# Optimization experiments

Measured on AMD Instinct MI355X. Metric: run time of the kernel, lower is better.

The kernel has to match this reference:

```python
import jax, jax.numpy as jnp
import numpy as np

HEADS = 16
KV_HEADS = 8
HEAD_DIM = 128
ROPE_BASE = 10000.0
RMS_EPS = 1e-5


def rmsnorm(x, w, eps=RMS_EPS):
    x = jnp.clip(x.astype(jnp.float32), -100.0, 100.0)
    var = jnp.clip(jnp.mean(x * x, axis=-1, keepdims=True), eps, None)
    x = x * jax.lax.rsqrt(var + eps)
    x = jnp.clip(x, -10.0, 10.0)
    return w * x


def activation_quant(x):
    x = jnp.clip(x, -50.0, 50.0)
    max_val = jnp.clip(jnp.max(jnp.abs(x), axis=-1, keepdims=True), 0.0001, None)
    scale = 127.0 / max_val
    return jnp.clip(jnp.round(x * scale), -128.0, 127.0) / scale


def weight_quant(w):
    scale = jnp.clip(jnp.mean(jnp.abs(w)), 1e-8, None)
    e = jnp.mean(w)
    return jnp.sign(w - e) * scale


def bitlinear(x, w, norm_w):
    xn = rmsnorm(x, norm_w)
    xq = xn + jax.lax.stop_gradient(activation_quant(xn) - xn)
    wq = w + jax.lax.stop_gradient(weight_quant(w) - w)
    return xq @ wq.T


def rope_tables(seq_len, dim):
    inv_freq = 1.0 / (ROPE_BASE ** (jnp.arange(0, dim, 2, dtype=jnp.float32) / dim))
    freqs = jnp.outer(jnp.arange(seq_len, dtype=jnp.float32), inv_freq)  # [S, dim/2]
    emb = jnp.concatenate([freqs, freqs], axis=-1)  # [S, dim]
    return jnp.cos(emb), jnp.sin(emb)


def rotate_half(x):
    x1, x2 = jnp.split(x, 2, axis=-1)
    return jnp.concatenate([-x2, x1], axis=-1)


def attention_forward(hidden_states, attention_mask, wq, wk, wv, wo, nq, nk, nv, no):
    B, S, H = hidden_states.shape
    q = bitlinear(hidden_states, wq, nq)  # [B,S,nh*hd]
    k = bitlinear(hidden_states, wk, nk)  # [B,S,nkv*hd]
    v = bitlinear(hidden_states, wv, nv)

    q = q.reshape(B, S, HEADS, HEAD_DIM).transpose(0, 2, 1, 3)       # [B,nh,S,hd]
    k = k.reshape(B, S, KV_HEADS, HEAD_DIM).transpose(0, 2, 1, 3)    # [B,nkv,S,hd]
    v = v.reshape(B, S, KV_HEADS, HEAD_DIM).transpose(0, 2, 1, 3)

    cos, sin = rope_tables(S, HEAD_DIM)
    cos = cos[None, None]  # [1,1,S,hd]
    sin = sin[None, None]
    q = q * cos + rotate_half(q) * sin
    k = k * cos + rotate_half(k) * sin

    groups = HEADS // KV_HEADS
    k_exp = jnp.repeat(k, groups, axis=1)  # [B,nh,S,hd]
    v_exp = jnp.repeat(v, groups, axis=1)

    scale = 1.0 / jnp.sqrt(jnp.float32(HEAD_DIM))
    scores = jnp.einsum('bhqd,bhkd->bhqk', q, k_exp) * scale
    scores = scores + attention_mask
    attn = jax.nn.softmax(scores, axis=-1)
    out = jnp.einsum('bhqk,bhkd->bhqd', attn, v_exp)
    out = out.transpose(0, 2, 1, 3).reshape(B, S, HEADS * HEAD_DIM)
    return bitlinear(out, wo, no)


def setup_inputs() -> dict:
    key = jax.random.key(0)
    ks = jax.random.split(key, 6)
    B, S, H = 2, 2048, 2048
    KVH = KV_HEADS * HEAD_DIM
    std = 0.02 / np.sqrt(H)
    return {
        'hidden_states': jax.random.normal(ks[0], (B, S, H), jnp.float32),
        'attention_mask': jnp.zeros((1, 1, S, S), jnp.float32),
        'wq': jax.random.normal(ks[1], (H, H), jnp.float32) * std,
        'wk': jax.random.normal(ks[2], (KVH, H), jnp.float32) * std,
        'wv': jax.random.normal(ks[3], (KVH, H), jnp.float32) * std,
        'wo': jax.random.normal(ks[4], (H, H), jnp.float32) * std,
        'nq': jnp.ones((H,), jnp.float32),
        'nk': jnp.ones((H,), jnp.float32),
        'nv': jnp.ones((H,), jnp.float32),
        'no': jnp.ones((H,), jnp.float32),
    }


def reference(hidden_states, attention_mask, wq, wk, wv, wo, nq, nk, nv, no):
    return attention_forward(hidden_states, attention_mask, wq, wk, wv, wo, nq, nk, nv, no)
```

## Files before the change

kernel.cpp:

```cpp
#include <hip/hip_runtime.h>


#define DI __device__ __forceinline__

using bf16   = __bf16;
using bf16x4 = __attribute__((ext_vector_type(4))) __bf16;
using bf16x8 = __attribute__((ext_vector_type(8))) __bf16;
using f32x4  = __attribute__((ext_vector_type(4))) float;
using i32x4  = __attribute__((ext_vector_type(4))) int;

DI void gl_lds16(void* lds, const void* g) {
  __builtin_amdgcn_global_load_lds((const __attribute__((address_space(1))) void*)g,
                                   (__attribute__((address_space(3))) void*)lds, 16, 0, 0);
}
DI float clampf(float x, float lo, float hi) { return fminf(fmaxf(x, lo), hi); }

template <int N> DI void wait_vm() {
  if constexpr (N == 8)      asm volatile("s_waitcnt vmcnt(8)" ::: "memory");
  else if constexpr (N == 6) asm volatile("s_waitcnt vmcnt(6)" ::: "memory");
  else if constexpr (N == 4) asm volatile("s_waitcnt vmcnt(4)" ::: "memory");
  else if constexpr (N == 3) asm volatile("s_waitcnt vmcnt(3)" ::: "memory");
  else                       asm volatile("s_waitcnt vmcnt(0)" ::: "memory");
}

DI float block_sum(float v, float* red, int lane, int w) {
#pragma unroll
  for (int o = 32; o > 0; o >>= 1) v += __shfl_xor(v, o, 64);
  __syncthreads();
  if (lane == 0) red[w] = v;
  __syncthreads();
  return red[0] + red[1] + red[2] + red[3];
}

__global__ void wstats_kernel(const float* wq, const float* wk, const float* wv,
                              const float* wo, float* stats) {
  __shared__ float red[4], red2[4];
  int t = threadIdx.x, lane = t & 63, w = t >> 6;
  int m = blockIdx.y;
  const float* src; int n4;
  if (m == 0)      { src = wq; n4 = 1048576; }
  else if (m == 1) { src = wk; n4 = 524288;  }
  else if (m == 2) { src = wv; n4 = 524288;  }
  else             { src = wo; n4 = 1048576; }
  float s = 0.f, sa = 0.f;
  for (int i = blockIdx.x * 256 + t; i < n4; i += 256 * 256) {
    float4 v = ((const float4*)src)[i];
    s  += v.x + v.y + v.z + v.w;
    sa += fabsf(v.x) + fabsf(v.y) + fabsf(v.z) + fabsf(v.w);
  }
#pragma unroll
  for (int o = 32; o > 0; o >>= 1) { s += __shfl_xor(s, o, 64); sa += __shfl_xor(sa, o, 64); }
  if (lane == 0) { red[w] = s; red2[w] = sa; }
  __syncthreads();
  if (t == 0) {
    atomicAdd(&stats[2 * m],     red[0] + red[1] + red[2] + red[3]);
    atomicAdd(&stats[2 * m + 1], red2[0] + red2[1] + red2[2] + red2[3]);
  }
}

__global__ void wsign_kernel(const float* wq, const float* wk, const float* wv, const float* wo,
                             char* sq, char* sk, char* sv, char* so,
                             const float* stats) {
  int m = blockIdx.y;
  const float* src; char* dst; int n4; float cinv;
  if (m == 0)      { src = wq; dst = sq; n4 = 1048576; cinv = 1.f / 4194304.f; }
  else if (m == 1) { src = wk; dst = sk; n4 = 524288;  cinv = 1.f / 2097152.f; }
  else if (m == 2) { src = wv; dst = sv; n4 = 524288;  cinv = 1.f / 2097152.f; }
  else             { src = wo; dst = so; n4 = 1048576; cinv = 1.f / 4194304.f; }
  float e = stats[2 * m] * cinv;
  for (int i = blockIdx.x * 256 + threadIdx.x; i < n4; i += 1024 * 256) {
    float4 v = ((const float4*)src)[i];
    char4 o;
    o.x = v.x > e ? 1 : (v.x < e ? -1 : 0);
    o.y = v.y > e ? 1 : (v.y < e ? -1 : 0);
    o.z = v.z > e ? 1 : (v.z < e ? -1 : 0);
    o.w = v.w > e ? 1 : (v.w < e ? -1 : 0);
    ((char4*)dst)[i] = o;
  }
}

__global__ void ropetab_kernel(float* ct, float* st) {
  int s = blockIdx.x, j = threadIdx.x;
  float invf = powf(10000.f, -(float)j * (1.f / 64.f));
  float a = (float)s * invf;
  ct[s * 64 + j] = cosf(a);
  st[s * 64 + j] = sinf(a);
}

template <int NW>
__launch_bounds__(256)
__global__ void rqnorm_kernel(const float* __restrict__ x,
                              const float* __restrict__ w0, const float* __restrict__ w1,
                              const float* __restrict__ w2,
                              char* a0, char* a1, char* a2,
                              float* r0, float* r1, float* r2) {
  __shared__ float red[4];
  __shared__ float redm[4][NW];
  int t = threadIdx.x, lane = t & 63, w = t >> 6;
  int row = blockIdx.x;
  const float* xr = x + (size_t)row * 2048;
  float4 u0 = ((const float4*)xr)[t * 2], u1 = ((const float4*)xr)[t * 2 + 1];
  float xs[8] = {u0.x, u0.y, u0.z, u0.w, u1.x, u1.y, u1.z, u1.w};
  float ss = 0.f;
#pragma unroll
  for (int e = 0; e < 8; ++e) { xs[e] = clampf(xs[e], -100.f, 100.f); ss += xs[e] * xs[e]; }
  float tot = block_sum(ss, red, lane, w);
  float var = fmaxf(tot * (1.f / 2048.f), 1e-5f);
  float inv = 1.f / sqrtf(var + 1e-5f);
#pragma unroll
  for (int e = 0; e < 8; ++e) xs[e] = clampf(xs[e] * inv, -10.f, 10.f);

  float y[NW][8], am[NW];
#pragma unroll
  for (int m = 0; m < NW; ++m) {
    const float* wt = (m == 0) ? w0 : (m == 1) ? w1 : w2;
    float4 b0 = ((const float4*)wt)[t * 2], b1 = ((const float4*)wt)[t * 2 + 1];
    float wv[8] = {b0.x, b0.y, b0.z, b0.w, b1.x, b1.y, b1.z, b1.w};
    am[m] = 0.f;
#pragma unroll
    for (int e = 0; e < 8; ++e) {
      y[m][e] = clampf(wv[e] * xs[e], -50.f, 50.f);
      am[m] = fmaxf(am[m], fabsf(y[m][e]));
    }
  }
#pragma unroll
  for (int o = 32; o > 0; o >>= 1)
#pragma unroll
    for (int m = 0; m < NW; ++m) am[m] = fmaxf(am[m], __shfl_xor(am[m], o, 64));
  if (lane == 0)
#pragma unroll
    for (int m = 0; m < NW; ++m) redm[w][m] = am[m];
  __syncthreads();
#pragma unroll
  for (int m = 0; m < NW; ++m) {
    char* a = (m == 0) ? a0 : (m == 1) ? a1 : a2;
    float* r = (m == 0) ? r0 : (m == 1) ? r1 : r2;
    float mx = fmaxf(fmaxf(redm[0][m], redm[1][m]), fmaxf(redm[2][m], redm[3][m]));
    float maxval = fmaxf(mx, 1e-4f);
    float sc = 127.f / maxval;
    union { char c[8]; int2 v; } pk;
#pragma unroll
    for (int e = 0; e < 8; ++e)
      pk.c[e] = (char)clampf(rintf(y[m][e] * sc), -128.f, 127.f);
    *(int2*)(a + (size_t)row * 2048 + t * 8) = pk.v;
    if (t == 0) r[row] = maxval * (1.f / 127.f);
  }
}

template <int BM, int BN>
DI void mm_pipe(const char* __restrict__ Ag0, const char* __restrict__ Bg0,
                char* As, char* Bs, int t, i32x4 (&acc)[BM / 64][BN / 32]) {
  constexpr int MR = BM / 64, NR = BN / 32;
  constexpr int AL = BM / 128, BL = BN / 128;
  constexpr int NT = 32;
  int lane = t & 63, l15 = lane & 15, quad = lane >> 4;
  int wv = t >> 6, wm = wv >> 1, wn = wv & 1;
  const char* agp[AL]; const char* bgp[BL];
#pragma unroll
  for (int i = 0; i < AL; ++i) {
    int c = t + i * 512, row = c >> 2, cr = c & 3;
    agp[i] = Ag0 + (size_t)row * 2048 + (cr ^ ((row >> 1) & 3)) * 16;
  }
#pragma unroll
  for (int i = 0; i < BL; ++i) {
    int c = t + i * 512, row = c >> 2, cr = c & 3;
    bgp[i] = Bg0 + (size_t)row * 2048 + (cr ^ ((row >> 1) & 3)) * 16;
  }
  auto stage = [&](int buf, int kt) {
    int kb = kt * 64;
#pragma unroll
    for (int i = 0; i < AL; ++i)
      gl_lds16(As + buf * (BM * 64) + (t + i * 512) * 16, agp[i] + kb);
#pragma unroll
    for (int i = 0; i < BL; ++i)
      gl_lds16(Bs + buf * (BN * 64) + (t + i * 512) * 16, bgp[i] + kb);
  };
  stage(0, 0);
  stage(1, 1);
  int arow = wm * (BM / 4) + l15;
  int brow = wn * (BN / 2) + l15;
  int sa = (arow >> 1) & 3, sb = (brow >> 1) & 3;
  int aco = (quad ^ sa) * 16, bco = (quad ^ sb) * 16;
  for (int kt = 0; kt < NT; ++kt) {
    int cur = kt & 1;
    if (kt == NT - 1) wait_vm<0>(); else wait_vm<AL + BL>();
    __builtin_amdgcn_sched_barrier(0);
    __builtin_amdgcn_s_barrier();
    __builtin_amdgcn_sched_barrier(0);
    const char* Ac = As + cur * (BM * 64);
    const char* Bc = Bs + cur * (BN * 64);
    __builtin_amdgcn_s_setprio(1);
    i32x4 af[MR], bfr[NR];
#pragma unroll
    for (int m = 0; m < MR; ++m)
      af[m] = *(const i32x4*)(Ac + (arow + m * 16) * 64 + aco);
#pragma unroll
    for (int n = 0; n < NR; ++n)
      bfr[n] = *(const i32x4*)(Bc + (brow + n * 16) * 64 + bco);
#pragma unroll
    for (int m = 0; m < MR; ++m)
#pragma unroll
      for (int n = 0; n < NR; ++n)
        acc[m][n] = __builtin_amdgcn_mfma_i32_16x16x64_i8(af[m], bfr[n], acc[m][n], 0, 0, 0);
    __builtin_amdgcn_s_setprio(0);
    __builtin_amdgcn_sched_barrier(0);
    __builtin_amdgcn_s_barrier();
    __builtin_amdgcn_sched_barrier(0);
    if (kt + 2 < NT) stage(cur, kt + 2);
  }
}

__launch_bounds__(512, 2)
__global__ void qkv_gemm(const char* __restrict__ Aq, const char* __restrict__ Ak,
                         const char* __restrict__ Av, const char* __restrict__ Ball,
                         const float* __restrict__ rq, const float* __restrict__ rk,
                         const float* __restrict__ rv, const float* __restrict__ stats,
                         bf16* __restrict__ qr, bf16* __restrict__ kr,
                         float* __restrict__ vlin,
                         const float* __restrict__ ct, const float* __restrict__ st) {
  __shared__ char As[2 * 256 * 64];
  __shared__ char Bs[2 * 256 * 64];
  int t = threadIdx.x;
  int bid = blockIdx.x;
  int swz = (bid & 7) * 32 + (bid >> 3);
  int x = swz >> 4, mt = swz & 15;
  int m0 = mt * 256;
  const char* A; const float* rs; float sw;
  if (x < 8)       { A = Aq; rs = rq; sw = stats[1] * (1.f / 4194304.f); }
  else if (x < 12) { A = Ak; rs = rk; sw = stats[3] * (1.f / 2097152.f); }
  else             { A = Av; rs = rv; sw = stats[5] * (1.f / 2097152.f); }
  sw = fmaxf(sw, 1e-8f);
  i32x4 acc[4][8] = {};
  mm_pipe<256, 256>(A + (size_t)m0 * 2048, Ball + (size_t)(x * 256) * 2048, As, Bs, t, acc);

  int lane = t & 63, l15 = lane & 15, quad = lane >> 4;
  int wv = t >> 6, wm = wv >> 1, wn = wv & 1;
  if (x < 12) {
    constexpr float QROPE = 0.08838834764831845f * 1.4426950408889634f;
    float qmul = (x < 8) ? QROPE : 1.f;
    bf16* outb = (x < 8) ? qr : kr;
    int h = (x < 8) ? (x * 2 + wn) : ((x - 8) * 2 + wn);
    int nh = (x < 8) ? 16 : 8;
#pragma unroll
    for (int m = 0; m < 4; ++m)
#pragma unroll
      for (int r = 0; r < 4; ++r) {
        int row = m0 + wm * 64 + m * 16 + quad * 4 + r;
        float rsc = rs[row] * sw * qmul;
        int s = row & 2047, b = row >> 11;
        size_t base = ((size_t)(b * nh + h) * 2048 + s) * 128;
#pragma unroll
        for (int n = 0; n < 4; ++n) {
          int d = n * 16 + l15;
          float x1 = (float)acc[m][n][r] * rsc;
          float x2 = (float)acc[m][n + 4][r] * rsc;
          float c = ct[s * 64 + d], sn = st[s * 64 + d];
          outb[base + d]      = (bf16)(x1 * c - x2 * sn);
          outb[base + d + 64] = (bf16)(x2 * c + x1 * sn);
        }
      }
  } else {
    int n0 = (x - 12) * 256 + wn * 128;
#pragma unroll
    for (int m = 0; m < 4; ++m)
#pragma unroll
      for (int r = 0; r < 4; ++r) {
        int row = m0 + wm * 64 + m * 16 + quad * 4 + r;
        float rsc = rs[row] * sw;
#pragma unroll
        for (int n = 0; n < 8; ++n)
          vlin[(size_t)row * 1024 + n0 + n * 16 + l15] = (float)acc[m][n][r] * rsc;
      }
  }
}

__launch_bounds__(512, 2)
__global__ void gemm_o(const char* __restrict__ A, const char* __restrict__ Bw,
                       const float* __restrict__ rs, const float* __restrict__ stats,
                       float* __restrict__ out) {
  __shared__ char As[2 * 128 * 64];
  __shared__ char Bs[2 * 256 * 64];
  int t = threadIdx.x;
  int bid = blockIdx.x;
  int swz = (bid & 7) * 32 + (bid >> 3);
  int x = swz & 7, mt = swz >> 3;
  int m0 = mt * 128, n0 = x * 256;
  i32x4 acc[2][8] = {};
  mm_pipe<128, 256>(A + (size_t)m0 * 2048, Bw + (size_t)n0 * 2048, As, Bs, t, acc);
  float sw = fmaxf(stats[7] * (1.f / 4194304.f), 1e-8f);
  int lane = t & 63, l15 = lane & 15, quad = lane >> 4;
  int wv = t >> 6, wm = wv >> 1, wn = wv & 1;
#pragma unroll
  for (int m = 0; m < 2; ++m)
#pragma unroll
    for (int r = 0; r < 4; ++r) {
      int row = m0 + wm * 32 + m * 16 + quad * 4 + r;
      float rsc = rs[row] * sw;
#pragma unroll
      for (int n = 0; n < 8; ++n)
        out[(size_t)row * 2048 + n0 + wn * 128 + n * 16 + l15] = (float)acc[m][n][r] * rsc;
    }
}

__global__ void vtrans_kernel(const float* __restrict__ v_lin, bf16* __restrict__ v_t) {
  __shared__ float tile[64][65];
  int t = threadIdx.x, c = t & 63, rq = t >> 6;
  int ct0 = blockIdx.x * 64, tt0 = blockIdx.y * 64;
#pragma unroll
  for (int i = 0; i < 16; ++i) {
    int r = rq * 16 + i;
    tile[r][c] = v_lin[(size_t)(tt0 + r) * 1024 + ct0 + c];
  }
  __syncthreads();
  int token = tt0 + c;
  int b = token >> 11, s = token & 2047;
#pragma unroll
  for (int i = 0; i < 16; ++i) {
    int cg = ct0 + rq * 16 + i;
    int kvh = cg >> 7, d = cg & 127;
    v_t[((size_t)(b * 8 + kvh) * 128 + d) * 2048 + s] = (bf16)tile[c][rq * 16 + i];
  }
}

__launch_bounds__(512, 4)
__global__ void attn_kernel(const bf16* __restrict__ Q, const bf16* __restrict__ Kc,
                            const bf16* __restrict__ Vt, const float* __restrict__ mask,
                            float* __restrict__ Oout) {
  constexpr float L2E  = 1.4426950408889634f;
  constexpr float DTHR = 8.f * L2E;
  __shared__ bf16 Ks[2][64 * 128];
  __shared__ bf16 Vs[2][128 * 64];
  __shared__ bf16 Ps[128 * 64];
  int t = threadIdx.x, w = t >> 6, lane = t & 63;
  int l15 = lane & 15, quad = lane >> 4;
  int bh = blockIdx.y, b = bh >> 4, h = bh & 15, kvh = h >> 1;
  int q0 = blockIdx.x * 128;
  const bf16* Qb = Q + (size_t)(b * 16 + h) * 2048 * 128;
  const bf16* Kb = Kc + (size_t)(b * 8 + kvh) * 2048 * 128;
  const bf16* Vb = Vt + (size_t)(b * 8 + kvh) * 128 * 2048;

  int qloc = w * 16 + l15;
  int qg = q0 + qloc;

  bf16x8 qf[4];
#pragma unroll
  for (int kc = 0; kc < 4; ++kc)
    qf[kc] = *(const bf16x8*)(Qb + (size_t)qg * 128 + kc * 32 + quad * 8);

  f32x4 Oa[8] = {};
  float mrow = -1e30f, lrow = 0.f;

  auto stage = [&](int buf, int kt) {
    int kk0 = kt * 64;
#pragma unroll
    for (int i = 0; i < 2; ++i) {
      int c = t + i * 512;
      int kr = c >> 4, c16 = c & 15;
      gl_lds16(&Ks[buf][c * 8],
               Kb + (size_t)(kk0 + kr) * 128 + ((c16 ^ (kr & 15)) * 8));
    }
#pragma unroll
    for (int i = 0; i < 2; ++i) {
      int c = t + i * 512;
      int vr = c >> 3, c8 = c & 7;
      gl_lds16(&Vs[buf][c * 8],
               Vb + (size_t)vr * 2048 + kk0 + ((c8 ^ (vr & 7)) * 8));
    }
  };

  stage(0, 0);

  f32x4 mv[4];
#pragma unroll
  for (int k2 = 0; k2 < 4; ++k2)
    mv[k2] = *(const f32x4*)(mask + (size_t)qg * 2048 + k2 * 16 + quad * 4);

  for (int kt = 0; kt < 32; ++kt) {
    int cur = kt & 1;
    __syncthreads();
    if (kt < 31) stage(cur ^ 1, kt + 1);

    f32x4 Sacc[4] = {};
    __builtin_amdgcn_s_setprio(1);
#pragma unroll
    for (int kc = 0; kc < 4; ++kc) {
      bf16x8 kf[4];
#pragma unroll
      for (int k2 = 0; k2 < 4; ++k2)
        kf[k2] = *(const bf16x8*)(&Ks[cur][(k2 * 16 + l15) * 128 + (((kc * 4 + quad) ^ l15) * 8)]);
#pragma unroll
      for (int k2 = 0; k2 < 4; ++k2)
        Sacc[k2] = __builtin_amdgcn_mfma_f32_16x16x32_bf16(kf[k2], qf[kc], Sacc[k2], 0, 0, 0);
    }
    __builtin_amdgcn_s_setprio(0);

#pragma unroll
    for (int k2 = 0; k2 < 4; ++k2)
#pragma unroll
      for (int r = 0; r < 4; ++r)
        Sacc[k2][r] = fmaf(mv[k2][r], L2E, Sacc[k2][r]);
    f32x4 vm;
#pragma unroll
    for (int r = 0; r < 4; ++r)
      vm[r] = fmaxf(fmaxf(Sacc[0][r], Sacc[1][r]), fmaxf(Sacc[2][r], Sacc[3][r]));
    float mx = fmaxf(fmaxf(vm[0], vm[1]), fmaxf(vm[2], vm[3]));
    mx = fmaxf(mx, __shfl_xor(mx, 16, 64));
    mx = fmaxf(mx, __shfl_xor(mx, 32, 64));
    if (!__all(mx <= mrow + DTHR)) {
      float mnew = fmaxf(mrow, mx);
      float alpha = exp2f(mrow - mnew);
      mrow = mnew;
      lrow *= alpha;
#pragma unroll
      for (int dt = 0; dt < 8; ++dt) Oa[dt] *= alpha;
    }
    f32x4 vs = {0.f, 0.f, 0.f, 0.f};
#pragma unroll
    for (int k2 = 0; k2 < 4; ++k2) {
      bf16x4 pk;
#pragma unroll
      for (int r = 0; r < 4; ++r) {
        float p = exp2f(Sacc[k2][r] - mrow);
        vs[r] += p;
        pk[r] = (bf16)p;
      }
      int c = k2 * 2 + (quad >> 1);
      *(bf16x4*)(&Ps[qloc * 64 + ((c ^ (qloc & 7)) * 8) + (quad & 1) * 4]) = pk;
    }
    float rsum = (vs[0] + vs[1]) + (vs[2] + vs[3]);
    rsum += __shfl_xor(rsum, 16, 64);
    rsum += __shfl_xor(rsum, 32, 64);
    lrow += rsum;

    if (kt < 31) {
      int kk1 = (kt + 1) * 64;
#pragma unroll
      for (int k2 = 0; k2 < 4; ++k2)
        mv[k2] = *(const f32x4*)(mask + (size_t)qg * 2048 + kk1 + k2 * 16 + quad * 4);
    }

    __builtin_amdgcn_s_setprio(1);
#pragma unroll
    for (int kc = 0; kc < 2; ++kc) {
      bf16x8 pf = *(const bf16x8*)(&Ps[qloc * 64 + (((kc * 4 + quad) ^ (l15 & 7)) * 8)]);
#pragma unroll
      for (int dt = 0; dt < 8; ++dt) {
        bf16x8 vf = *(const bf16x8*)(&Vs[cur][(dt * 16 + l15) * 64 +
                                              (((kc * 4 + quad) ^ (l15 & 7)) * 8)]);
        Oa[dt] = __builtin_amdgcn_mfma_f32_16x16x32_bf16(vf, pf, Oa[dt], 0, 0, 0);
      }
    }
    __builtin_amdgcn_s_setprio(0);
  }

  float inv = 1.f / lrow;
  int token = b * 2048 + qg;
#pragma unroll
  for (int dt = 0; dt < 8; ++dt) {
    f32x4 o = Oa[dt] * inv;
    *(f32x4*)(Oout + (size_t)token * 2048 + h * 128 + dt * 16 + quad * 4) = o;
  }
}

extern "C" void kernel_launch(void* const* d_in, const int* in_sizes, int n_in,
                              void* d_out, int out_size, void* d_ws, size_t ws_size,
                              hipStream_t stream) {
  const float* hidden = (const float*)d_in[0];
  const float* mask   = (const float*)d_in[1];
  const float* wq = (const float*)d_in[2];
  const float* wk = (const float*)d_in[3];
  const float* wv = (const float*)d_in[4];
  const float* wo = (const float*)d_in[5];
  const float* nq = (const float*)d_in[6];
  const float* nk = (const float*)d_in[7];
  const float* nv = (const float*)d_in[8];
  const float* no = (const float*)d_in[9];
  float* out = (float*)d_out;
  char* ws = (char*)d_ws;

  constexpr size_t O_STATS = 0;
  constexpr size_t O_CT    = 256;
  constexpr size_t O_ST    = O_CT  + 524288;
  constexpr size_t O_SQ    = O_ST  + 524288;
  constexpr size_t O_SK    = O_SQ  + 4194304;
  constexpr size_t O_SV    = O_SK  + 2097152;
  constexpr size_t O_SO    = O_SV  + 2097152;
  constexpr size_t O_RSQ   = O_SO  + 4194304;
  constexpr size_t O_RSK   = O_RSQ + 16384;
  constexpr size_t O_RSV   = O_RSK + 16384;
  constexpr size_t O_RSO   = O_RSV + 16384;
  constexpr size_t O_AQQ   = O_RSO + 16384;
  constexpr size_t O_AQK   = O_AQQ + 8388608;
  constexpr size_t O_AQV   = O_AQK + 8388608;
  constexpr size_t O_QR    = O_AQV + 8388608;
  constexpr size_t O_KR    = O_QR  + 16777216;
  constexpr size_t O_VT    = O_KR  + 8388608;
  constexpr size_t O_VLIN2 = O_VT  + 8388608;
  constexpr size_t O_ATTN  = O_VLIN2 + 16777216;
  constexpr size_t O_AQO   = O_AQQ;

  float* stats = (float*)(ws + O_STATS);
  float* ct = (float*)(ws + O_CT);
  float* st = (float*)(ws + O_ST);

  (void)hipMemsetAsync(ws + O_STATS, 0, 256, stream);

  wstats_kernel<<<dim3(256, 4), 256, 0, stream>>>(wq, wk, wv, wo, stats);
  wsign_kernel<<<dim3(1024, 4), 256, 0, stream>>>(wq, wk, wv, wo,
      ws + O_SQ, ws + O_SK, ws + O_SV, ws + O_SO, stats);
  ropetab_kernel<<<dim3(2048), 64, 0, stream>>>(ct, st);

  rqnorm_kernel<3><<<dim3(4096), 256, 0, stream>>>(hidden, nq, nk, nv,
      ws + O_AQQ, ws + O_AQK, ws + O_AQV,
      (float*)(ws + O_RSQ), (float*)(ws + O_RSK), (float*)(ws + O_RSV));

  qkv_gemm<<<dim3(256), 512, 0, stream>>>(
      ws + O_AQQ, ws + O_AQK, ws + O_AQV, ws + O_SQ,
      (const float*)(ws + O_RSQ), (const float*)(ws + O_RSK), (const float*)(ws + O_RSV),
      stats, (bf16*)(ws + O_QR), (bf16*)(ws + O_KR), (float*)(ws + O_VLIN2), ct, st);

  vtrans_kernel<<<dim3(16, 64), 256, 0, stream>>>((const float*)(ws + O_VLIN2), (bf16*)(ws + O_VT));

  attn_kernel<<<dim3(16, 32), 512, 0, stream>>>(
      (const bf16*)(ws + O_QR), (const bf16*)(ws + O_KR), (const bf16*)(ws + O_VT),
      mask, (float*)(ws + O_ATTN));

  rqnorm_kernel<1><<<dim3(4096), 256, 0, stream>>>((const float*)(ws + O_ATTN), no, no, no,
      ws + O_AQO, ws + O_AQO, ws + O_AQO,
      (float*)(ws + O_RSO), (float*)(ws + O_RSO), (float*)(ws + O_RSO));

  gemm_o<<<dim3(256), 512, 0, stream>>>(
      ws + O_AQO, ws + O_SO, (float*)(ws + O_RSO), stats, out);

  (void)in_sizes; (void)n_in; (void)out_size; (void)ws_size;
}
```

Baseline: 376.7 us.

## Fuse V transpose into QKV GEMM, merge rope tables, widen GEMM K tile

The QKV GEMM epilogue now writes V directly as transposed bf16, removing the separate vtrans kernel and its fp32 intermediate buffer. Rope table generation moves into an extra grid row of the weight-stats kernel, saving one launch. The int8 GEMM pipeline doubles its K step per stage to 128 bytes with a wider XOR swizzle, halving the number of barriers. This raises shared memory per block, which may reduce occupancy, and the transposed V stores are strided.

Measured after the change: 367.6 us (median of 2 runs). -2.4%, faster.

```diff
diff --git a/kernel.cpp b/kernel.cpp
--- a/kernel.cpp
+++ b/kernel.cpp
@@ -19,7 +19,6 @@
   if constexpr (N == 8)      asm volatile("s_waitcnt vmcnt(8)" ::: "memory");
   else if constexpr (N == 6) asm volatile("s_waitcnt vmcnt(6)" ::: "memory");
   else if constexpr (N == 4) asm volatile("s_waitcnt vmcnt(4)" ::: "memory");
-  else if constexpr (N == 3) asm volatile("s_waitcnt vmcnt(3)" ::: "memory");
   else                       asm volatile("s_waitcnt vmcnt(0)" ::: "memory");
 }
 
@@ -33,10 +32,24 @@
 }
 
 __global__ void wstats_kernel(const float* wq, const float* wk, const float* wv,
-                              const float* wo, float* stats) {
+                              const float* wo, float* stats, float* ct, float* st) {
+  int t = threadIdx.x;
+  int m = blockIdx.y;
+  if (m == 4) {
+    int idx = blockIdx.x * 256 + t;
+#pragma unroll
+    for (int k = 0; k < 2; ++k) {
+      int e = idx + k * 65536;
+      int s = e >> 6, j = e & 63;
+      float invf = powf(10000.f, -(float)j * (1.f / 64.f));
+      float a = (float)s * invf;
+      ct[s * 64 + j] = cosf(a);
+      st[s * 64 + j] = sinf(a);
+    }
+    return;
+  }
   __shared__ float red[4], red2[4];
-  int t = threadIdx.x, lane = t & 63, w = t >> 6;
-  int m = blockIdx.y;
+  int lane = t & 63, w = t >> 6;
   const float* src; int n4;
   if (m == 0)      { src = wq; n4 = 1048576; }
   else if (m == 1) { src = wk; n4 = 524288;  }
@@ -79,14 +92,6 @@
   }
 }
 
-__global__ void ropetab_kernel(float* ct, float* st) {
-  int s = blockIdx.x, j = threadIdx.x;
-  float invf = powf(10000.f, -(float)j * (1.f / 64.f));
-  float a = (float)s * invf;
-  ct[s * 64 + j] = cosf(a);
-  st[s * 64 + j] = sinf(a);
-}
-
 template <int NW>
 __launch_bounds__(256)
 __global__ void rqnorm_kernel(const float* __restrict__ x,
@@ -151,57 +156,61 @@
 DI void mm_pipe(const char* __restrict__ Ag0, const char* __restrict__ Bg0,
                 char* As, char* Bs, int t, i32x4 (&acc)[BM / 64][BN / 32]) {
   constexpr int MR = BM / 64, NR = BN / 32;
-  constexpr int AL = BM / 128, BL = BN / 128;
-  constexpr int NT = 32;
+  constexpr int AL = BM / 64, BL = BN / 64;
+  constexpr int NT = 16;
   int lane = t & 63, l15 = lane & 15, quad = lane >> 4;
   int wv = t >> 6, wm = wv >> 1, wn = wv & 1;
   const char* agp[AL]; const char* bgp[BL];
 #pragma unroll
   for (int i = 0; i < AL; ++i) {
-    int c = t + i * 512, row = c >> 2, cr = c & 3;
-    agp[i] = Ag0 + (size_t)row * 2048 + (cr ^ ((row >> 1) & 3)) * 16;
+    int c = t + i * 512, row = c >> 3, cr = c & 7;
+    agp[i] = Ag0 + (size_t)row * 2048 + (cr ^ (row & 7)) * 16;
   }
 #pragma unroll
   for (int i = 0; i < BL; ++i) {
-    int c = t + i * 512, row = c >> 2, cr = c & 3;
-    bgp[i] = Bg0 + (size_t)row * 2048 + (cr ^ ((row >> 1) & 3)) * 16;
+    int c = t + i * 512, row = c >> 3, cr = c & 7;
+    bgp[i] = Bg0 + (size_t)row * 2048 + (cr ^ (row & 7)) * 16;
   }
   auto stage = [&](int buf, int kt) {
-    int kb = kt * 64;
+    int kb = kt * 128;
 #pragma unroll
     for (int i = 0; i < AL; ++i)
-      gl_lds16(As + buf * (BM * 64) + (t + i * 512) * 16, agp[i] + kb);
+      gl_lds16(As + buf * (BM * 128) + (t + i * 512) * 16, agp[i] + kb);
 #pragma unroll
     for (int i = 0; i < BL; ++i)
-      gl_lds16(Bs + buf * (BN * 64) + (t + i * 512) * 16, bgp[i] + kb);
+      gl_lds16(Bs + buf * (BN * 128) + (t + i * 512) * 16, bgp[i] + kb);
   };
   stage(0, 0);
   stage(1, 1);
   int arow = wm * (BM / 4) + l15;
   int brow = wn * (BN / 2) + l15;
-  int sa = (arow >> 1) & 3, sb = (brow >> 1) & 3;
-  int aco = (quad ^ sa) * 16, bco = (quad ^ sb) * 16;
+  int sa = arow & 7, sb = brow & 7;
   for (int kt = 0; kt < NT; ++kt) {
     int cur = kt & 1;
     if (kt == NT - 1) wait_vm<0>(); else wait_vm<AL + BL>();
     __builtin_amdgcn_sched_barrier(0);
     __builtin_amdgcn_s_barrier();
     __builtin_amdgcn_sched_barrier(0);
-    const char* Ac = As + cur * (BM * 64);
-    const char* Bc = Bs + cur * (BN * 64);
+    const char* Ac = As + cur * (BM * 128);
+    const char* Bc = Bs + cur * (BN * 128);
     __builtin_amdgcn_s_setprio(1);
-    i32x4 af[MR], bfr[NR];
-#pragma unroll
-    for (int m = 0; m < MR; ++m)
-      af[m] = *(const i32x4*)(Ac + (arow + m * 16) * 64 + aco);
-#pragma unroll
-    for (int n = 0; n < NR; ++n)
-      bfr[n] = *(const i32x4*)(Bc + (brow + n * 16) * 64 + bco);
-#pragma unroll
-    for (int m = 0; m < MR; ++m)
+#pragma unroll
+    for (int ks = 0; ks < 2; ++ks) {
+      int aco = ((ks * 4 + quad) ^ sa) * 16;
+      int bco = ((ks * 4 + quad) ^ sb) * 16;
+      i32x4 af[MR], bfr[NR];
+#pragma unroll
+      for (int m = 0; m < MR; ++m)
+        af[m] = *(const i32x4*)(Ac + (arow + m * 16) * 128 + aco);
 #pragma unroll
       for (int n = 0; n < NR; ++n)
-        acc[m][n] = __builtin_amdgcn_mfma_i32_16x16x64_i8(af[m], bfr[n], acc[m][n], 0, 0, 0);
+        bfr[n] = *(const i32x4*)(Bc + (brow + n * 16) * 128 + bco);
+#pragma unroll
+      for (int m = 0; m < MR; ++m)
+#pragma unroll
+        for (int n = 0; n < NR; ++n)
+          acc[m][n] = __builtin_amdgcn_mfma_i32_16x16x64_i8(af[m], bfr[n], acc[m][n], 0, 0, 0);
+    }
     __builtin_amdgcn_s_setprio(0);
     __builtin_amdgcn_sched_barrier(0);
     __builtin_amdgcn_s_barrier();
@@ -216,10 +225,10 @@
                          const float* __restrict__ rq, const float* __restrict__ rk,
                          const float* __restrict__ rv, const float* __restrict__ stats,
                          bf16* __restrict__ qr, bf16* __restrict__ kr,
-                         float* __restrict__ vlin,
+                         bf16* __restrict__ vt,
                          const float* __restrict__ ct, const float* __restrict__ st) {
-  __shared__ char As[2 * 256 * 64];
-  __shared__ char Bs[2 * 256 * 64];
+  __shared__ char As[2 * 256 * 128];
+  __shared__ char Bs[2 * 256 * 128];
   int t = threadIdx.x;
   int bid = blockIdx.x;
   int swz = (bid & 7) * 32 + (bid >> 3);
@@ -260,16 +269,22 @@
         }
       }
   } else {
-    int n0 = (x - 12) * 256 + wn * 128;
+    int n0g = (x - 12) * 256 + wn * 128;
+    int kvh = n0g >> 7;
+    int btok = m0 >> 11;
+    int s0 = (m0 & 2047) + wm * 64 + quad * 4;
 #pragma unroll
     for (int m = 0; m < 4; ++m)
 #pragma unroll
-      for (int r = 0; r < 4; ++r) {
-        int row = m0 + wm * 64 + m * 16 + quad * 4 + r;
-        float rsc = rs[row] * sw;
-#pragma unroll
-        for (int n = 0; n < 8; ++n)
-          vlin[(size_t)row * 1024 + n0 + n * 16 + l15] = (float)acc[m][n][r] * rsc;
+      for (int n = 0; n < 8; ++n) {
+        int d = n * 16 + l15;
+        bf16x4 pk;
+#pragma unroll
+        for (int r = 0; r < 4; ++r) {
+          int row = m0 + wm * 64 + m * 16 + quad * 4 + r;
+          pk[r] = (bf16)((float)acc[m][n][r] * (rs[row] * sw));
+        }
+        *(bf16x4*)(vt + ((size_t)(btok * 8 + kvh) * 128 + d) * 2048 + s0 + m * 16) = pk;
       }
   }
 }
@@ -278,8 +293,8 @@
 __global__ void gemm_o(const char* __restrict__ A, const char* __restrict__ Bw,
                        const float* __restrict__ rs, const float* __restrict__ stats,
                        float* __restrict__ out) {
-  __shared__ char As[2 * 128 * 64];
-  __shared__ char Bs[2 * 256 * 64];
+  __shared__ char As[2 * 128 * 128];
+  __shared__ char Bs[2 * 256 * 128];
   int t = threadIdx.x;
   int bid = blockIdx.x;
   int swz = (bid & 7) * 32 + (bid >> 3);
@@ -300,26 +315,6 @@
       for (int n = 0; n < 8; ++n)
         out[(size_t)row * 2048 + n0 + wn * 128 + n * 16 + l15] = (float)acc[m][n][r] * rsc;
     }
-}
-
-__global__ void vtrans_kernel(const float* __restrict__ v_lin, bf16* __restrict__ v_t) {
-  __shared__ float tile[64][65];
-  int t = threadIdx.x, c = t & 63, rq = t >> 6;
-  int ct0 = blockIdx.x * 64, tt0 = blockIdx.y * 64;
-#pragma unroll
-  for (int i = 0; i < 16; ++i) {
-    int r = rq * 16 + i;
-    tile[r][c] = v_lin[(size_t)(tt0 + r) * 1024 + ct0 + c];
-  }
-  __syncthreads();
-  int token = tt0 + c;
-  int b = token >> 11, s = token & 2047;
-#pragma unroll
-  for (int i = 0; i < 16; ++i) {
-    int cg = ct0 + rq * 16 + i;
-    int kvh = cg >> 7, d = cg & 127;
-    v_t[((size_t)(b * 8 + kvh) * 128 + d) * 2048 + s] = (bf16)tile[c][rq * 16 + i];
-  }
 }
 
 __launch_bounds__(512, 4)
@@ -495,8 +490,7 @@
   constexpr size_t O_QR    = O_AQV + 8388608;
   constexpr size_t O_KR    = O_QR  + 16777216;
   constexpr size_t O_VT    = O_KR  + 8388608;
-  constexpr size_t O_VLIN2 = O_VT  + 8388608;
-  constexpr size_t O_ATTN  = O_VLIN2 + 16777216;
+  constexpr size_t O_ATTN  = O_VT  + 8388608;
   constexpr size_t O_AQO   = O_AQQ;
 
   float* stats = (float*)(ws + O_STATS);
@@ -505,10 +499,9 @@
 
   (void)hipMemsetAsync(ws + O_STATS, 0, 256, stream);
 
-  wstats_kernel<<<dim3(256, 4), 256, 0, stream>>>(wq, wk, wv, wo, stats);
+  wstats_kernel<<<dim3(256, 5), 256, 0, stream>>>(wq, wk, wv, wo, stats, ct, st);
   wsign_kernel<<<dim3(1024, 4), 256, 0, stream>>>(wq, wk, wv, wo,
       ws + O_SQ, ws + O_SK, ws + O_SV, ws + O_SO, stats);
-  ropetab_kernel<<<dim3(2048), 64, 0, stream>>>(ct, st);
 
   rqnorm_kernel<3><<<dim3(4096), 256, 0, stream>>>(hidden, nq, nk, nv,
       ws + O_AQQ, ws + O_AQK, ws + O_AQV,
@@ -517,9 +510,7 @@
   qkv_gemm<<<dim3(256), 512, 0, stream>>>(
       ws + O_AQQ, ws + O_AQK, ws + O_AQV, ws + O_SQ,
       (const float*)(ws + O_RSQ), (const float*)(ws + O_RSK), (const float*)(ws + O_RSV),
-      stats, (bf16*)(ws + O_QR), (bf16*)(ws + O_KR), (float*)(ws + O_VLIN2), ct, st);
-
-  vtrans_kernel<<<dim3(16, 64), 256, 0, stream>>>((const float*)(ws + O_VLIN2), (bf16*)(ws + O_VT));
+      stats, (bf16*)(ws + O_QR), (bf16*)(ws + O_KR), (bf16*)(ws + O_VT), ct, st);
 
   attn_kernel<<<dim3(16, 32), 512, 0, stream>>>(
       (const bf16*)(ws + O_QR), (const bf16*)(ws + O_KR), (const bf16*)(ws + O_VT),
```
